# Kernel tuning notes

Hardware: AMD Instinct MI355X
Metric: run time of the kernel (lower is better)

## Reference

```python
import jax, jax.numpy as jnp
import numpy as np

BETA = 0.001  # l2 regularization coefficient from __init__
N_SEG = 4096


def _pair_indices(cu):
    # Build global pair index arrays (pos<neg within each segment),
    # equivalent to torch.combinations(arange(L), 2) per segment.
    cache = {}
    pos_l, neg_l, seg_l = [], [], []
    for s in range(len(cu) - 1):
        a, b = int(cu[s]), int(cu[s + 1])
        L = b - a
        if L not in cache:
            cache[L] = np.triu_indices(L, 1)
        i, j = cache[L]
        pos_l.append(a + i)
        neg_l.append(a + j)
        seg_l.append(np.full(i.shape[0], s, dtype=np.int64))
    pos = np.concatenate(pos_l).astype(np.int64)
    neg = np.concatenate(neg_l).astype(np.int64)
    seg = np.concatenate(seg_l)
    counts = np.bincount(seg, minlength=len(cu) - 1).astype(np.float32)
    return pos, neg, seg, counts


def setup_inputs() -> dict:
    key = jax.random.key(0)
    rng = np.random.default_rng(0)
    lengths = rng.integers(32, 128, N_SEG)  # variable candidates per prompt
    cu = np.concatenate([[0], np.cumsum(lengths)]).astype(np.int64)
    n = int(cu[-1])
    logits = jax.random.normal(key, (n,), dtype=jnp.float32)
    return {"logits": logits, "cu_lengths": jnp.asarray(cu)}


def reference(logits, cu_lengths):
    cu = np.asarray(jax.device_get(cu_lengths))  # boundaries are static ints
    pos_idx, neg_idx, seg_id, counts = _pair_indices(cu)
    pos_idx = jnp.asarray(pos_idx)
    neg_idx = jnp.asarray(neg_idx)
    seg_id = jnp.asarray(seg_id)
    counts = jnp.asarray(counts)

    pos = logits[pos_idx]  # [P]
    neg = logits[neg_idx]  # [P]
    l2 = 0.5 * (pos * pos + neg * neg)
    pair_loss = -jax.nn.log_sigmoid(pos - neg) + BETA * l2  # [P]
    # per-segment mean, then mean over segments (reduction='mean')
    seg_sum = jax.ops.segment_sum(pair_loss, seg_id, num_segments=len(cu) - 1)
    per_seg = seg_sum / counts
    return jnp.mean(per_seg)
```

## Files before the change

### kernel.cpp

```cpp
#include <hip/hip_runtime.h>
#include <math.h>

#define BETA 0.001f
#define WPB  4

__global__ __launch_bounds__(WPB * 64) void rmloss_kernel(
    const float* __restrict__ logits,
    const int*   __restrict__ cu,
    float*       __restrict__ out,
    int n_seg, float inv_n)
{
    const int wave = threadIdx.x >> 6;
    const int lane = threadIdx.x & 63;
    const int s = blockIdx.x * WPB + wave;

    __shared__ float xs[WPB][128];
    __shared__ float wsum[WPB];

    const float kNL2E = -1.44269504088896340736f;
    const float kT2L2 =  1.38629436111989061883f;

    float segval = 0.0f;

    if (s < n_seg) {
        const int a   = cu[s];
        const int L   = cu[s + 1] - a;
        const int Lm1 = L - 1;

        float* __restrict__ x = xs[wave];

        const bool a_ok = lane < L;
        const bool b_ok = lane + 64 < L;
        const float va = a_ok ? logits[a + lane] : 0.0f;
        const float vb = b_ok ? logits[a + lane + 64] : 0.0f;
        x[lane]      = va;
        x[lane + 64] = vb;
        __builtin_amdgcn_wave_barrier();

        float su_a = 0.0f, p_a = 1.0f;
        float su_b = 0.0f, p_b = 1.0f;

        if (L > 64) {
            #pragma unroll 4
            for (int j = 0; j < L; ++j) {
                const float v = x[j];
                const float ua = fabsf(va - v);
                const float ea = __builtin_amdgcn_exp2f(ua * kNL2E);
                su_a += ua;
                p_a  *= 1.0f + ea;
                const float ub = fabsf(vb - v);
                const float eb = __builtin_amdgcn_exp2f(ub * kNL2E);
                su_b += ub;
                p_b  *= 1.0f + eb;
            }
        } else {
            #pragma unroll 4
            for (int j = 0; j < L; ++j) {
                const float v = x[j];
                const float ua = fabsf(va - v);
                const float ea = __builtin_amdgcn_exp2f(ua * kNL2E);
                su_a += ua;
                p_a  *= 1.0f + ea;
            }
        }

        const float ha = su_a + kT2L2 * __builtin_amdgcn_logf(p_a);
        const float hb = su_b + kT2L2 * __builtin_amdgcn_logf(p_b);
        const float acch = (a_ok ? ha : 0.0f) + (b_ok ? hb : 0.0f);

        const float lin = va * (float)(2 * lane - Lm1)
                        + vb * (float)(2 * (lane + 64) - Lm1);
        const float sq  = va * va + vb * vb;

        float f = 0.25f * acch + 0.5f * lin + (0.5f * BETA * (float)Lm1) * sq;
        #pragma unroll
        for (int off = 32; off > 0; off >>= 1)
            f += __shfl_down(f, off, 64);

        if (lane == 0) {
            const float P    = 0.5f * (float)(L * Lm1);
            const float diag = 0.25f * (float)L * kT2L2;
            segval = (f - diag) / P * inv_n;
        }
    }

    if (lane == 0) wsum[wave] = segval;
    __syncthreads();
    if (threadIdx.x == 0) {
        atomicAdd(out, wsum[0] + wsum[1] + wsum[2] + wsum[3]);
    }
}

extern "C" void kernel_launch(void* const* d_in, const int* in_sizes, int n_in,
                              void* d_out, int out_size, void* d_ws, size_t ws_size,
                              hipStream_t stream) {
    (void)n_in; (void)out_size; (void)d_ws; (void)ws_size;

    const float* logits = (const float*)d_in[0];
    const int*   cu     = (const int*)d_in[1];
    float*       out    = (float*)d_out;

    const int n_seg  = in_sizes[1] - 1;
    const int blocks = (n_seg + WPB - 1) / WPB;

    hipMemsetAsync(out, 0, sizeof(float), stream);
    rmloss_kernel<<<blocks, WPB * 64, 0, stream>>>(logits, cu, out, n_seg,
                                                   1.0f / (float)n_seg);
}
```

Before: 72.15 us.

## Broadcast values via readlane, replace atomics and memset with two-pass reduction

The pairwise inner loop now takes each element straight from a register with readlane instead of staging logits in LDS, and folds the product update into an fma. The single atomicAdd per block and the memset are replaced by writing per-segment partials to workspace, followed by a one-block reduction kernel. This removes the LDS traffic, the block barrier and atomic contention, at the cost of a second kernel launch and a serial one-block reduction over 4096 partials.

```diff
diff --git a/kernel.cpp b/kernel.cpp
--- a/kernel.cpp
+++ b/kernel.cpp
@@ -4,106 +4,129 @@
 #define BETA 0.001f
 #define WPB  4
 
-__global__ __launch_bounds__(WPB * 64) void rmloss_kernel(
+
+__device__ __forceinline__ float lane_bcast(float v, int lane_u) {
+    return __uint_as_float(
+        (unsigned)__builtin_amdgcn_readlane((int)__float_as_uint(v), lane_u));
+}
+
+__global__ __launch_bounds__(WPB * 64) void rmloss_part(
     const float* __restrict__ logits,
     const int*   __restrict__ cu,
-    float*       __restrict__ out,
+    float*       __restrict__ part,
     int n_seg, float inv_n)
 {
     const int wave = threadIdx.x >> 6;
     const int lane = threadIdx.x & 63;
     const int s = blockIdx.x * WPB + wave;
+    if (s >= n_seg) return;
 
-    __shared__ float xs[WPB][128];
-    __shared__ float wsum[WPB];
+    const int a   = cu[s];
+    const int L   = cu[s + 1] - a;
+    const int Lm1 = L - 1;
 
     const float kNL2E = -1.44269504088896340736f;
     const float kT2L2 =  1.38629436111989061883f;
 
-    float segval = 0.0f;
+    const bool a_ok = lane < L;
+    const bool b_ok = lane + 64 < L;
+    const float va = a_ok ? logits[a + lane] : 0.0f;
+    const float vb = b_ok ? logits[a + lane + 64] : 0.0f;
 
-    if (s < n_seg) {
-        const int a   = cu[s];
-        const int L   = cu[s + 1] - a;
-        const int Lm1 = L - 1;
+    float su_a = 0.0f, p_a = 1.0f;
+    float su_b = 0.0f, p_b = 1.0f;
 
-        float* __restrict__ x = xs[wave];
-
-        const bool a_ok = lane < L;
-        const bool b_ok = lane + 64 < L;
-        const float va = a_ok ? logits[a + lane] : 0.0f;
-        const float vb = b_ok ? logits[a + lane + 64] : 0.0f;
-        x[lane]      = va;
-        x[lane + 64] = vb;
-        __builtin_amdgcn_wave_barrier();
-
-        float su_a = 0.0f, p_a = 1.0f;
-        float su_b = 0.0f, p_b = 1.0f;
-
-        if (L > 64) {
-            #pragma unroll 4
-            for (int j = 0; j < L; ++j) {
-                const float v = x[j];
-                const float ua = fabsf(va - v);
-                const float ea = __builtin_amdgcn_exp2f(ua * kNL2E);
-                su_a += ua;
-                p_a  *= 1.0f + ea;
-                const float ub = fabsf(vb - v);
-                const float eb = __builtin_amdgcn_exp2f(ub * kNL2E);
-                su_b += ub;
-                p_b  *= 1.0f + eb;
-            }
-        } else {
-            #pragma unroll 4
-            for (int j = 0; j < L; ++j) {
-                const float v = x[j];
-                const float ua = fabsf(va - v);
-                const float ea = __builtin_amdgcn_exp2f(ua * kNL2E);
-                su_a += ua;
-                p_a  *= 1.0f + ea;
-            }
+    if (L > 64) {
+        #pragma unroll 4
+        for (int j = 0; j < 64; ++j) {
+            const float v  = lane_bcast(va, j);
+            const float ua = fabsf(va - v);
+            su_a += ua;
+            p_a = fmaf(p_a, __builtin_amdgcn_exp2f(ua * kNL2E), p_a);
+            const float ub = fabsf(vb - v);
+            su_b += ub;
+            p_b = fmaf(p_b, __builtin_amdgcn_exp2f(ub * kNL2E), p_b);
         }
-
-        const float ha = su_a + kT2L2 * __builtin_amdgcn_logf(p_a);
-        const float hb = su_b + kT2L2 * __builtin_amdgcn_logf(p_b);
-        const float acch = (a_ok ? ha : 0.0f) + (b_ok ? hb : 0.0f);
-
-        const float lin = va * (float)(2 * lane - Lm1)
-                        + vb * (float)(2 * (lane + 64) - Lm1);
-        const float sq  = va * va + vb * vb;
-
-        float f = 0.25f * acch + 0.5f * lin + (0.5f * BETA * (float)Lm1) * sq;
-        #pragma unroll
-        for (int off = 32; off > 0; off >>= 1)
-            f += __shfl_down(f, off, 64);
-
-        if (lane == 0) {
-            const float P    = 0.5f * (float)(L * Lm1);
-            const float diag = 0.25f * (float)L * kT2L2;
-            segval = (f - diag) / P * inv_n;
+        const int t2 = L - 64;
+        #pragma unroll 4
+        for (int j = 0; j < t2; ++j) {
+            const float v  = lane_bcast(vb, j);
+            const float ua = fabsf(va - v);
+            su_a += ua;
+            p_a = fmaf(p_a, __builtin_amdgcn_exp2f(ua * kNL2E), p_a);
+            const float ub = fabsf(vb - v);
+            su_b += ub;
+            p_b = fmaf(p_b, __builtin_amdgcn_exp2f(ub * kNL2E), p_b);
+        }
+    } else {
+        #pragma unroll 4
+        for (int j = 0; j < L; ++j) {
+            const float v  = lane_bcast(va, j);
+            const float ua = fabsf(va - v);
+            su_a += ua;
+            p_a = fmaf(p_a, __builtin_amdgcn_exp2f(ua * kNL2E), p_a);
         }
     }
 
-    if (lane == 0) wsum[wave] = segval;
+    const float ha = su_a + kT2L2 * __builtin_amdgcn_logf(p_a);
+    const float hb = su_b + kT2L2 * __builtin_amdgcn_logf(p_b);
+    const float acch = (a_ok ? ha : 0.0f) + (b_ok ? hb : 0.0f);
+
+    const float lin = va * (float)(2 * lane - Lm1)
+                    + vb * (float)(2 * (lane + 64) - Lm1);
+    const float sq  = va * va + vb * vb;
+
+    float f = 0.25f * acch + 0.5f * lin + (0.5f * BETA * (float)Lm1) * sq;
+    #pragma unroll
+    for (int off = 32; off > 0; off >>= 1)
+        f += __shfl_down(f, off, 64);
+
+    if (lane == 0) {
+        const float P    = 0.5f * (float)(L * Lm1);
+        const float diag = 0.25f * (float)L * kT2L2;
+        part[s] = (f - diag) / P * inv_n;
+    }
+}
+
+__global__ __launch_bounds__(256) void rmloss_reduce(
+    const float* __restrict__ part, float* __restrict__ out, int n)
+{
+    const int t = threadIdx.x;
+    float acc = 0.0f;
+
+    const int n4 = n >> 2;
+    const float4* __restrict__ p4 = (const float4*)part;
+    for (int i = t; i < n4; i += 256) {
+        const float4 v = p4[i];
+        acc += (v.x + v.y) + (v.z + v.w);
+    }
+    for (int i = (n4 << 2) + t; i < n; i += 256)
+        acc += part[i];
+
+    #pragma unroll
+    for (int off = 32; off > 0; off >>= 1)
+        acc += __shfl_down(acc, off, 64);
+
+    __shared__ float ws[4];
+    if ((t & 63) == 0) ws[t >> 6] = acc;
     __syncthreads();
-    if (threadIdx.x == 0) {
-        atomicAdd(out, wsum[0] + wsum[1] + wsum[2] + wsum[3]);
-    }
+    if (t == 0) out[0] = (ws[0] + ws[1]) + (ws[2] + ws[3]);
 }
 
 extern "C" void kernel_launch(void* const* d_in, const int* in_sizes, int n_in,
                               void* d_out, int out_size, void* d_ws, size_t ws_size,
                               hipStream_t stream) {
-    (void)n_in; (void)out_size; (void)d_ws; (void)ws_size;
+    (void)n_in; (void)out_size; (void)ws_size;
 
     const float* logits = (const float*)d_in[0];
     const int*   cu     = (const int*)d_in[1];
     float*       out    = (float*)d_out;
+    float*       part   = (float*)d_ws;
 
     const int n_seg  = in_sizes[1] - 1;
     const int blocks = (n_seg + WPB - 1) / WPB;
 
-    hipMemsetAsync(out, 0, sizeof(float), stream);
-    rmloss_kernel<<<blocks, WPB * 64, 0, stream>>>(logits, cu, out, n_seg,
-                                                   1.0f / (float)n_seg);
+    rmloss_part<<<blocks, WPB * 64, 0, stream>>>(logits, cu, part, n_seg,
+                                                 1.0f / (float)n_seg);
+    rmloss_reduce<<<1, 256, 0, stream>>>(part, out, n_seg);
 }
```

After: 70.55 us. -2.2%, faster.
